# Performance work log

Hardware: AMD Instinct MI355X
Metric: run time of the kernel (lower is better)

The kernel has to match this reference:

```python
import jax, jax.numpy as jnp
import numpy as np

N_HEAD = 16


def setup_inputs() -> dict:
    key = jax.random.key(0)
    ks = jax.random.split(key, 4)
    B, S, E = 1, 4096, 1024
    x = jax.random.normal(ks[0], (B, S, E), dtype=jnp.float32)
    # causal mask: True where attention is DISALLOWED (upper triangle)
    masked_matrix = ~jnp.tril(jnp.ones((S, S), dtype=bool))[None, None]
    Wqkv = jax.random.normal(ks[1], (E, 3 * E), dtype=jnp.float32) * (1.0 / np.sqrt(E))
    bqkv = jnp.zeros((3 * E,), dtype=jnp.float32)
    Wp = jax.random.normal(ks[2], (E, E), dtype=jnp.float32) * (1.0 / np.sqrt(E))
    bp = jnp.zeros((E,), dtype=jnp.float32)
    return {"x": x, "masked_matrix": masked_matrix, "Wqkv": Wqkv, "bqkv": bqkv,
            "Wp": Wp, "bp": bp}


def reference(x, masked_matrix, Wqkv, bqkv, Wp, bp):
    B, S, E = x.shape
    H = N_HEAD
    D = E // H
    qkv = x @ Wqkv + bqkv                        # [B,S,3E]
    q, k, v = jnp.split(qkv, 3, axis=-1)
    q = q.reshape(B, S, H, D).transpose(0, 2, 1, 3)  # [B,H,S,D]
    k = k.reshape(B, S, H, D).transpose(0, 2, 1, 3)
    v = v.reshape(B, S, H, D).transpose(0, 2, 1, 3)
    # NOTE: source applies NO 1/sqrt(D) scaling — kept faithful.
    att = jnp.einsum('bhqd,bhkd->bhqk', q, k)    # [B,H,S,S]
    att = jnp.where(masked_matrix, jnp.float32(-jnp.inf), att)
    att = jax.nn.softmax(att, axis=-1)
    res = jnp.einsum('bhqk,bhkd->bhqd', att, v)  # [B,H,S,D]
    res = res.transpose(0, 2, 1, 3).reshape(B, S, E)
    return res @ Wp + bp
```

## Files before the change

### kernel.cpp

```cpp
#include <hip/hip_runtime.h>
#include <hip/hip_bf16.h>
#include <math.h>

#define S_LEN 4096
#define EMB   1024
#define NHEAD 16
#define HDIM  64

typedef __attribute__((ext_vector_type(8))) _Float16 half8;
typedef __attribute__((ext_vector_type(4))) _Float16 half4;
typedef __attribute__((ext_vector_type(4))) float float4_t;

#define GLOBAL_AS(p) ((const __attribute__((address_space(1))) void*)(p))
#define LDS_AS(p)    ((__attribute__((address_space(3))) void*)(p))

#define LOG2E 1.4426950408889634f

__global__ __launch_bounds__(256) void prep(
    const float* __restrict__ x, const float* __restrict__ Wqkv,
    const float* __restrict__ Wp,
    _Float16* __restrict__ xh, _Float16* __restrict__ WTh,
    _Float16* __restrict__ WpT)
{
    const int bid = blockIdx.x;
    if (bid < 4096) {
        const int i = bid * 256 + threadIdx.x;
        const float4_t v = ((const float4_t*)x)[i];
        half4 hh;
#pragma unroll
        for (int j = 0; j < 4; ++j) hh[j] = (_Float16)v[j];
        ((half4*)xh)[i] = hh;
        return;
    }
    __shared__ float t[64][65];
    const float* in;
    _Float16* out;
    int R, C, bx, by;
    if (bid < 4096 + 768) {
        const int idx = bid - 4096;
        bx = idx % 48; by = idx / 48;
        in = Wqkv; out = WTh; R = 1024; C = 3072;
    } else {
        const int idx = bid - 4864;
        bx = idx & 15; by = idx >> 4;
        in = Wp; out = WpT; R = 1024; C = 1024;
    }
    const int r0 = by * 64, c0 = bx * 64;
    for (int i = threadIdx.x; i < 64 * 64; i += 256) {
        int r = i >> 6, c = i & 63;
        t[r][c] = in[(size_t)(r0 + r) * C + c0 + c];
    }
    __syncthreads();
    for (int i = threadIdx.x; i < 64 * 64; i += 256) {
        int c = i >> 6, r = i & 63;
        out[(size_t)(c0 + c) * R + r0 + r] = (_Float16)t[r][c];
    }
}

__global__ __launch_bounds__(256) void gemm_qkv(
    const _Float16* __restrict__ Ag, const _Float16* __restrict__ Bg,
    const float* __restrict__ bias,
    _Float16* __restrict__ qk, _Float16* __restrict__ vt, int K)
{
    constexpr int BK = 32;
    __shared__ _Float16 Ah[128 * BK];
    __shared__ _Float16 Bh[128 * BK];

    const int tid = threadIdx.x;
    const int wave = tid >> 6, lane = tid & 63;
    const int l16 = lane & 15, quad = lane >> 4;
    const int wr = wave >> 1, wc = wave & 1;
    const int row0 = blockIdx.y * 128, col0 = blockIdx.x * 128;
    const int lrow = lane >> 2, lc8 = (lane & 3) * 8;

    float4_t acc[4][4];
#pragma unroll
    for (int i = 0; i < 4; ++i)
#pragma unroll
        for (int j = 0; j < 4; ++j) acc[i][j] = (float4_t){0.f, 0.f, 0.f, 0.f};

    for (int k0 = 0; k0 < K; k0 += BK) {
        __syncthreads();
#pragma unroll
        for (int i = 0; i < 2; ++i) {
            const int ar = i * 64 + wave * 16;
            __builtin_amdgcn_global_load_lds(
                GLOBAL_AS(Ag + (size_t)(row0 + ar + lrow) * K + k0 + lc8),
                LDS_AS(&Ah[ar * BK]), 16, 0, 0);
            __builtin_amdgcn_global_load_lds(
                GLOBAL_AS(Bg + (size_t)(col0 + ar + lrow) * K + k0 + lc8),
                LDS_AS(&Bh[ar * BK]), 16, 0, 0);
        }
        __syncthreads();

        half8 af[4], bfr[4];
#pragma unroll
        for (int t = 0; t < 4; ++t) {
            af[t]  = *(const half8*)&Ah[(wr * 64 + t * 16 + l16) * BK + quad * 8];
            bfr[t] = *(const half8*)&Bh[(wc * 64 + t * 16 + l16) * BK + quad * 8];
        }
#pragma unroll
        for (int i = 0; i < 4; ++i)
#pragma unroll
            for (int j = 0; j < 4; ++j)
                acc[i][j] = __builtin_amdgcn_mfma_f32_16x16x32_f16(af[i], bfr[j], acc[i][j], 0, 0, 0);
    }

#pragma unroll
    for (int i = 0; i < 4; ++i) {
#pragma unroll
        for (int j = 0; j < 4; ++j) {
            const int colb = col0 + wc * 64 + j * 16 + l16;
            const float bv = bias[colb];
            const int rowb = row0 + wr * 64 + i * 16 + quad * 4;
            if (colb < 2048) {
                const float sc = (colb >= 1024) ? LOG2E : 1.0f;
#pragma unroll
                for (int r = 0; r < 4; ++r)
                    qk[(size_t)(rowb + r) * 2048 + colb] =
                        (_Float16)((acc[i][j][r] + bv) * sc);
            } else {
                half4 w;
#pragma unroll
                for (int r = 0; r < 4; ++r) w[r] = (_Float16)(acc[i][j][r] + bv);
                *(half4*)&vt[(size_t)(colb - 2048) * 4096 + rowb] = w;
            }
        }
    }
}

__global__ __launch_bounds__(256) void gemm_out(
    const _Float16* __restrict__ Ag, const _Float16* __restrict__ Bg,
    const float* __restrict__ bias, float* __restrict__ C, int N, int K)
{
    constexpr int BK = 32;
    __shared__ _Float16 Ah[128 * BK];
    __shared__ _Float16 Bh[64 * BK];

    const int tid = threadIdx.x;
    const int wave = tid >> 6, lane = tid & 63;
    const int l16 = lane & 15, quad = lane >> 4;
    const int row0 = blockIdx.y * 128, col0 = blockIdx.x * 64;
    const int lrow = lane >> 2, lc8 = (lane & 3) * 8;

    float4_t acc[2][4];
#pragma unroll
    for (int i = 0; i < 2; ++i)
#pragma unroll
        for (int j = 0; j < 4; ++j) acc[i][j] = (float4_t){0.f, 0.f, 0.f, 0.f};

    for (int k0 = 0; k0 < K; k0 += BK) {
        __syncthreads();
#pragma unroll
        for (int i = 0; i < 2; ++i) {
            const int ar = i * 64 + wave * 16;
            __builtin_amdgcn_global_load_lds(
                GLOBAL_AS(Ag + (size_t)(row0 + ar + lrow) * K + k0 + lc8),
                LDS_AS(&Ah[ar * BK]), 16, 0, 0);
        }
        {
            const int br = wave * 16;
            __builtin_amdgcn_global_load_lds(
                GLOBAL_AS(Bg + (size_t)(col0 + br + lrow) * K + k0 + lc8),
                LDS_AS(&Bh[br * BK]), 16, 0, 0);
        }
        __syncthreads();

        half8 af[2], bfr[4];
#pragma unroll
        for (int t = 0; t < 2; ++t)
            af[t] = *(const half8*)&Ah[(wave * 32 + t * 16 + l16) * BK + quad * 8];
#pragma unroll
        for (int t = 0; t < 4; ++t)
            bfr[t] = *(const half8*)&Bh[(t * 16 + l16) * BK + quad * 8];
#pragma unroll
        for (int i = 0; i < 2; ++i)
#pragma unroll
            for (int j = 0; j < 4; ++j)
                acc[i][j] = __builtin_amdgcn_mfma_f32_16x16x32_f16(af[i], bfr[j], acc[i][j], 0, 0, 0);
    }

#pragma unroll
    for (int i = 0; i < 2; ++i) {
#pragma unroll
        for (int j = 0; j < 4; ++j) {
            const int colb = col0 + j * 16 + l16;
            const float bv = bias[colb];
#pragma unroll
            for (int r = 0; r < 4; ++r) {
                const int row = row0 + wave * 32 + i * 16 + quad * 4 + r;
                C[(size_t)row * N + colb] = acc[i][j][r] + bv;
            }
        }
    }
}

__global__ __launch_bounds__(256, 4) void flash_attn_f16(
    const _Float16* __restrict__ qk, const _Float16* __restrict__ v_t,
    _Float16* __restrict__ resh)
{
    __shared__ __align__(16) _Float16 KsT[2][64 * 64];
    __shared__ __align__(16) _Float16 VtT[2][64 * 64];
    __shared__ __align__(16) _Float16 Pb[4][16][76];

    const int bid  = blockIdx.x;
    const int h    = (bid & 7) * 2 + ((bid >> 3) & 1);
    const int tile = 63 - (bid >> 4);
    const int wave = threadIdx.x >> 6;
    const int lane = threadIdx.x & 63;
    const int l16  = lane & 15;
    const int quad = lane >> 4;

    const int dma_r = wave * 16 + (lane >> 3);
    const int dma_c = ((lane & 7) ^ (lane >> 3)) * 8;

    const _Float16* kplane = qk + 1024 + h * HDIM;
    const _Float16* vplane = v_t + (size_t)h * HDIM * 4096;

    const int q0      = tile * 64 + wave * 16;
    const int kb_last = tile * 64;

    const size_t qoff = (size_t)(q0 + l16) * 2048 + h * HDIM + quad * 8;
    half8 qf0 = *(const half8*)(qk + qoff);
    half8 qf1 = *(const half8*)(qk + qoff + 32);

    float4_t o[4];
#pragma unroll
    for (int c = 0; c < 4; ++c) o[c] = (float4_t){0.f, 0.f, 0.f, 0.f};
    float m_r = -INFINITY, l_r = 0.f;

#pragma unroll
    for (int p = 0; p < 2; ++p) {
        const int r = dma_r + p * 8;
        __builtin_amdgcn_global_load_lds(
            GLOBAL_AS(kplane + (size_t)r * 2048 + dma_c),
            LDS_AS(&KsT[0][(wave * 128 + p * 64) * 8]), 16, 0, 0);
        __builtin_amdgcn_global_load_lds(
            GLOBAL_AS(vplane + (size_t)r * 4096 + dma_c),
            LDS_AS(&VtT[0][(wave * 128 + p * 64) * 8]), 16, 0, 0);
    }

    int ib = 0;
    for (int kb = 0; kb <= kb_last; kb += 64, ib ^= 1) {
        __syncthreads();

        if (kb < kb_last) {
            const int kn = kb + 64;
#pragma unroll
            for (int p = 0; p < 2; ++p) {
                const int r = dma_r + p * 8;
                __builtin_amdgcn_global_load_lds(
                    GLOBAL_AS(kplane + (size_t)(kn + r) * 2048 + dma_c),
                    LDS_AS(&KsT[ib ^ 1][(wave * 128 + p * 64) * 8]), 16, 0, 0);
                __builtin_amdgcn_global_load_lds(
                    GLOBAL_AS(vplane + (size_t)r * 4096 + kn + dma_c),
                    LDS_AS(&VtT[ib ^ 1][(wave * 128 + p * 64) * 8]), 16, 0, 0);
            }
        }

        float4_t s[4];
#pragma unroll
        for (int t = 0; t < 4; ++t) {
            const int row = t * 16 + l16;
            const int r7 = row & 7;
            half8 a0 = *(const half8*)&KsT[ib][(row * 8 + (quad ^ r7)) * 8];
            half8 a1 = *(const half8*)&KsT[ib][(row * 8 + ((quad + 4) ^ r7)) * 8];
            float4_t a = (float4_t){0.f, 0.f, 0.f, 0.f};
            a = __builtin_amdgcn_mfma_f32_16x16x32_f16(a0, qf0, a, 0, 0, 0);
            a = __builtin_amdgcn_mfma_f32_16x16x32_f16(a1, qf1, a, 0, 0, 0);
            s[t] = a;
        }

        if (kb + 63 > q0) {
            const int qg = q0 + l16;
#pragma unroll
            for (int t = 0; t < 4; ++t)
#pragma unroll
                for (int r = 0; r < 4; ++r) {
                    const int key = kb + t * 16 + quad * 4 + r;
                    if (key > qg) s[t][r] = -INFINITY;
                }
        }

        float mx = s[0][0];
#pragma unroll
        for (int t = 0; t < 4; ++t)
#pragma unroll
            for (int r = 0; r < 4; ++r) mx = fmaxf(mx, s[t][r]);
        mx = fmaxf(mx, __shfl_xor(mx, 16));
        mx = fmaxf(mx, __shfl_xor(mx, 32));
        const float mnew  = fmaxf(m_r, mx);
        const float alpha = __builtin_amdgcn_exp2f(m_r - mnew);

        float p[4][4];
        float sum = 0.f;
#pragma unroll
        for (int t = 0; t < 4; ++t)
#pragma unroll
            for (int r = 0; r < 4; ++r) {
                p[t][r] = __builtin_amdgcn_exp2f(s[t][r] - mnew);
                sum += p[t][r];
            }
        sum += __shfl_xor(sum, 16);
        sum += __shfl_xor(sum, 32);
        l_r = l_r * alpha + sum;
        m_r = mnew;
#pragma unroll
        for (int ct = 0; ct < 4; ++ct)
#pragma unroll
            for (int r = 0; r < 4; ++r) o[ct][r] *= alpha;

#pragma unroll
        for (int t = 0; t < 4; ++t) {
            half4 w;
#pragma unroll
            for (int r = 0; r < 4; ++r) w[r] = (_Float16)p[t][r];
            *(half4*)&Pb[wave][l16][t * 16 + quad * 4] = w;
        }
        half8 pb0 = *(const half8*)&Pb[wave][l16][quad * 8];
        half8 pb1 = *(const half8*)&Pb[wave][l16][32 + quad * 8];

#pragma unroll
        for (int ct = 0; ct < 4; ++ct) {
            const int row = ct * 16 + l16;
            const int r7 = row & 7;
            half8 va0 = *(const half8*)&VtT[ib][(row * 8 + (quad ^ r7)) * 8];
            half8 va1 = *(const half8*)&VtT[ib][(row * 8 + ((quad + 4) ^ r7)) * 8];
            o[ct] = __builtin_amdgcn_mfma_f32_16x16x32_f16(va0, pb0, o[ct], 0, 0, 0);
            o[ct] = __builtin_amdgcn_mfma_f32_16x16x32_f16(va1, pb1, o[ct], 0, 0, 0);
        }
    }

    const float inv = 1.0f / l_r;
#pragma unroll
    for (int ct = 0; ct < 4; ++ct) {
        half4 w;
#pragma unroll
        for (int r = 0; r < 4; ++r) w[r] = (_Float16)(o[ct][r] * inv);
        *(half4*)&resh[(size_t)(q0 + l16) * EMB + h * HDIM + ct * 16 + quad * 4] = w;
    }
}

extern "C" void kernel_launch(void* const* d_in, const int* in_sizes, int n_in,
                              void* d_out, int out_size, void* d_ws, size_t ws_size,
                              hipStream_t stream)
{
    const float* x    = (const float*)d_in[0];
    const float* Wqkv = (const float*)d_in[2];
    const float* bqkv = (const float*)d_in[3];
    const float* Wp   = (const float*)d_in[4];
    const float* bp   = (const float*)d_in[5];
    float* out = (float*)d_out;

    _Float16* xh  = (_Float16*)d_ws;
    _Float16* WTh = xh + (size_t)4096 * 1024;
    _Float16* qkh = WTh + (size_t)3072 * 1024;
    _Float16* vtg = qkh + (size_t)4096 * 2048;
    _Float16* WpT = vtg + (size_t)1024 * 4096;
    _Float16* resh = xh;

    dim3 blk(256);

    prep<<<dim3(5120), blk, 0, stream>>>(x, Wqkv, Wp, xh, WTh, WpT);

    gemm_qkv<<<dim3(3072 / 128, 4096 / 128), blk, 0, stream>>>(
        xh, WTh, bqkv, qkh, vtg, 1024);

    flash_attn_f16<<<dim3(1024), dim3(256), 0, stream>>>(qkh, vtg, resh);

    gemm_out<<<dim3(1024 / 64, 4096 / 128), blk, 0, stream>>>(
        resh, WpT, bp, out, 1024, 1024);
}
```

Measured before the change: 260.5 us.

## Replace LDS P staging with bpermute, lazy rescale, deferred row-sum reduction

Removes the per-wave LDS buffer used to transpose P into MFMA B-operand layout. It uses ds_bpermute shuffles with packed f16 conversion instead, which frees LDS so occupancy can rise to 5 blocks per SM. It also skips rescaling the O accumulator unless the running max grows by more than a threshold, and defers the cross-lane sum reduction to the end. The lazy max threshold risks fp16 overflow in P (values up to 2^8) and changes rounding behaviour via round-toward-zero conversion.

```diff
diff --git a/kernel.cpp b/kernel.cpp
--- a/kernel.cpp
+++ b/kernel.cpp
@@ -9,7 +9,9 @@
 
 typedef __attribute__((ext_vector_type(8))) _Float16 half8;
 typedef __attribute__((ext_vector_type(4))) _Float16 half4;
+typedef __attribute__((ext_vector_type(2))) _Float16 half2_t;
 typedef __attribute__((ext_vector_type(4))) float float4_t;
+typedef __attribute__((ext_vector_type(4))) int int4_t;
 
 #define GLOBAL_AS(p) ((const __attribute__((address_space(1))) void*)(p))
 #define LDS_AS(p)    ((__attribute__((address_space(3))) void*)(p))
@@ -195,13 +197,12 @@
     }
 }
 
-__global__ __launch_bounds__(256, 4) void flash_attn_f16(
+__global__ __launch_bounds__(256, 5) void flash_attn_f16(
     const _Float16* __restrict__ qk, const _Float16* __restrict__ v_t,
     _Float16* __restrict__ resh)
 {
     __shared__ __align__(16) _Float16 KsT[2][64 * 64];
     __shared__ __align__(16) _Float16 VtT[2][64 * 64];
-    __shared__ __align__(16) _Float16 Pb[4][16][76];
 
     const int bid  = blockIdx.x;
     const int h    = (bid & 7) * 2 + ((bid >> 3) & 1);
@@ -213,6 +214,10 @@
 
     const int dma_r = wave * 16 + (lane >> 3);
     const int dma_c = ((lane & 7) ^ (lane >> 3)) * 8;
+
+    const int srcA4 = (l16 + ((quad & 1) << 5)) << 2;
+    const int srcB4 = srcA4 + 64;
+    const bool hiT  = quad >= 2;
 
     const _Float16* kplane = qk + 1024 + h * HDIM;
     const _Float16* vplane = v_t + (size_t)h * HDIM * 4096;
@@ -282,43 +287,70 @@
                 }
         }
 
-        float mx = s[0][0];
-#pragma unroll
-        for (int t = 0; t < 4; ++t)
-#pragma unroll
-            for (int r = 0; r < 4; ++r) mx = fmaxf(mx, s[t][r]);
+        const float t0m = fmaxf(fmaxf(s[0][0], s[0][1]), fmaxf(s[0][2], s[0][3]));
+        const float t1m = fmaxf(fmaxf(s[1][0], s[1][1]), fmaxf(s[1][2], s[1][3]));
+        const float t2m = fmaxf(fmaxf(s[2][0], s[2][1]), fmaxf(s[2][2], s[2][3]));
+        const float t3m = fmaxf(fmaxf(s[3][0], s[3][1]), fmaxf(s[3][2], s[3][3]));
+        float mx = fmaxf(fmaxf(t0m, t1m), fmaxf(t2m, t3m));
         mx = fmaxf(mx, __shfl_xor(mx, 16));
         mx = fmaxf(mx, __shfl_xor(mx, 32));
-        const float mnew  = fmaxf(m_r, mx);
+        const bool  grow  = mx > m_r + 8.0f;
+        const float mnew  = grow ? mx : m_r;
         const float alpha = __builtin_amdgcn_exp2f(m_r - mnew);
 
         float p[4][4];
-        float sum = 0.f;
+        float lsum = 0.f;
 #pragma unroll
         for (int t = 0; t < 4; ++t)
 #pragma unroll
             for (int r = 0; r < 4; ++r) {
                 p[t][r] = __builtin_amdgcn_exp2f(s[t][r] - mnew);
-                sum += p[t][r];
+                lsum += p[t][r];
             }
-        sum += __shfl_xor(sum, 16);
-        sum += __shfl_xor(sum, 32);
-        l_r = l_r * alpha + sum;
+        l_r = l_r * alpha + lsum;
         m_r = mnew;
-#pragma unroll
-        for (int ct = 0; ct < 4; ++ct)
-#pragma unroll
-            for (int r = 0; r < 4; ++r) o[ct][r] *= alpha;
-
+        if (__any(grow)) {
+#pragma unroll
+            for (int ct = 0; ct < 4; ++ct)
+#pragma unroll
+                for (int r = 0; r < 4; ++r) o[ct][r] *= alpha;
+        }
+
+        int w[4][2];
 #pragma unroll
         for (int t = 0; t < 4; ++t) {
-            half4 w;
-#pragma unroll
-            for (int r = 0; r < 4; ++r) w[r] = (_Float16)p[t][r];
-            *(half4*)&Pb[wave][l16][t * 16 + quad * 4] = w;
-        }
-        half8 pb0 = *(const half8*)&Pb[wave][l16][quad * 8];
-        half8 pb1 = *(const half8*)&Pb[wave][l16][32 + quad * 8];
+            w[t][0] = __builtin_bit_cast(int, __builtin_amdgcn_cvt_pkrtz(p[t][0], p[t][1]));
+            w[t][1] = __builtin_bit_cast(int, __builtin_amdgcn_cvt_pkrtz(p[t][2], p[t][3]));
+        }
+        int4_t v0, v1;
+        {
+            const int a0 = __builtin_amdgcn_ds_bpermute(srcA4, w[0][0]);
+            const int a1 = __builtin_amdgcn_ds_bpermute(srcA4, w[1][0]);
+            v0[0] = hiT ? a1 : a0;
+            const int b0 = __builtin_amdgcn_ds_bpermute(srcA4, w[0][1]);
+            const int b1 = __builtin_amdgcn_ds_bpermute(srcA4, w[1][1]);
+            v0[1] = hiT ? b1 : b0;
+            const int c0 = __builtin_amdgcn_ds_bpermute(srcB4, w[0][0]);
+            const int c1 = __builtin_amdgcn_ds_bpermute(srcB4, w[1][0]);
+            v0[2] = hiT ? c1 : c0;
+            const int d0 = __builtin_amdgcn_ds_bpermute(srcB4, w[0][1]);
+            const int d1 = __builtin_amdgcn_ds_bpermute(srcB4, w[1][1]);
+            v0[3] = hiT ? d1 : d0;
+            const int e0 = __builtin_amdgcn_ds_bpermute(srcA4, w[2][0]);
+            const int e1 = __builtin_amdgcn_ds_bpermute(srcA4, w[3][0]);
+            v1[0] = hiT ? e1 : e0;
+            const int f0 = __builtin_amdgcn_ds_bpermute(srcA4, w[2][1]);
+            const int f1 = __builtin_amdgcn_ds_bpermute(srcA4, w[3][1]);
+            v1[1] = hiT ? f1 : f0;
+            const int g0 = __builtin_amdgcn_ds_bpermute(srcB4, w[2][0]);
+            const int g1 = __builtin_amdgcn_ds_bpermute(srcB4, w[3][0]);
+            v1[2] = hiT ? g1 : g0;
+            const int h0 = __builtin_amdgcn_ds_bpermute(srcB4, w[2][1]);
+            const int h1 = __builtin_amdgcn_ds_bpermute(srcB4, w[3][1]);
+            v1[3] = hiT ? h1 : h0;
+        }
+        const half8 pb0 = __builtin_bit_cast(half8, v0);
+        const half8 pb1 = __builtin_bit_cast(half8, v1);
 
 #pragma unroll
         for (int ct = 0; ct < 4; ++ct) {
@@ -331,7 +363,9 @@
         }
     }
 
-    const float inv = 1.0f / l_r;
+    float lr = l_r + __shfl_xor(l_r, 16);
+    lr += __shfl_xor(lr, 32);
+    const float inv = 1.0f / lr;
 #pragma unroll
     for (int ct = 0; ct < 4; ++ct) {
         half4 w;
```

Result: slower. 270.2 us (+3.7%).

## Use 128-query attention tiles with 8 waves, lazy rescaling and deferred row-sum

Applied to the files above, without the earlier changes.

Doubles the attention block to 512 threads covering 128 queries, so each K/V tile loaded into LDS is shared by eight waves instead of four, halving per-block DMA work per wave. Waves skip key blocks that lie entirely beyond their causal range. Adds a lazy max update (rescale only when the new max exceeds the old one by more than 8) and moves the cross-lane row-sum reduction to the end of the kernel. The trade-off is fewer blocks, idle waves on skipped blocks near the diagonal, and possible fp16 overflow of P when the stale max lags by up to 8 in log2 units.

```diff
diff --git a/kernel.cpp b/kernel.cpp
--- a/kernel.cpp
+++ b/kernel.cpp
@@ -195,30 +195,30 @@
     }
 }
 
-__global__ __launch_bounds__(256, 4) void flash_attn_f16(
+__global__ __launch_bounds__(512, 4) void flash_attn_f16(
     const _Float16* __restrict__ qk, const _Float16* __restrict__ v_t,
     _Float16* __restrict__ resh)
 {
     __shared__ __align__(16) _Float16 KsT[2][64 * 64];
     __shared__ __align__(16) _Float16 VtT[2][64 * 64];
-    __shared__ __align__(16) _Float16 Pb[4][16][76];
+    __shared__ __align__(16) _Float16 Pb[8][16][76];
 
     const int bid  = blockIdx.x;
     const int h    = (bid & 7) * 2 + ((bid >> 3) & 1);
-    const int tile = 63 - (bid >> 4);
+    const int tile = 31 - (bid >> 4);
     const int wave = threadIdx.x >> 6;
     const int lane = threadIdx.x & 63;
     const int l16  = lane & 15;
     const int quad = lane >> 4;
 
-    const int dma_r = wave * 16 + (lane >> 3);
+    const int dma_r = wave * 8 + (lane >> 3);
     const int dma_c = ((lane & 7) ^ (lane >> 3)) * 8;
 
     const _Float16* kplane = qk + 1024 + h * HDIM;
     const _Float16* vplane = v_t + (size_t)h * HDIM * 4096;
 
-    const int q0      = tile * 64 + wave * 16;
-    const int kb_last = tile * 64;
+    const int q0      = tile * 128 + wave * 16;
+    const int kb_last = tile * 128 + 64;
 
     const size_t qoff = (size_t)(q0 + l16) * 2048 + h * HDIM + quad * 8;
     half8 qf0 = *(const half8*)(qk + qoff);
@@ -229,15 +229,13 @@
     for (int c = 0; c < 4; ++c) o[c] = (float4_t){0.f, 0.f, 0.f, 0.f};
     float m_r = -INFINITY, l_r = 0.f;
 
-#pragma unroll
-    for (int p = 0; p < 2; ++p) {
-        const int r = dma_r + p * 8;
+    {
         __builtin_amdgcn_global_load_lds(
-            GLOBAL_AS(kplane + (size_t)r * 2048 + dma_c),
-            LDS_AS(&KsT[0][(wave * 128 + p * 64) * 8]), 16, 0, 0);
+            GLOBAL_AS(kplane + (size_t)dma_r * 2048 + dma_c),
+            LDS_AS(&KsT[0][(wave * 64) * 8]), 16, 0, 0);
         __builtin_amdgcn_global_load_lds(
-            GLOBAL_AS(vplane + (size_t)r * 4096 + dma_c),
-            LDS_AS(&VtT[0][(wave * 128 + p * 64) * 8]), 16, 0, 0);
+            GLOBAL_AS(vplane + (size_t)dma_r * 4096 + dma_c),
+            LDS_AS(&VtT[0][(wave * 64) * 8]), 16, 0, 0);
     }
 
     int ib = 0;
@@ -246,92 +244,93 @@
 
         if (kb < kb_last) {
             const int kn = kb + 64;
-#pragma unroll
-            for (int p = 0; p < 2; ++p) {
-                const int r = dma_r + p * 8;
-                __builtin_amdgcn_global_load_lds(
-                    GLOBAL_AS(kplane + (size_t)(kn + r) * 2048 + dma_c),
-                    LDS_AS(&KsT[ib ^ 1][(wave * 128 + p * 64) * 8]), 16, 0, 0);
-                __builtin_amdgcn_global_load_lds(
-                    GLOBAL_AS(vplane + (size_t)r * 4096 + kn + dma_c),
-                    LDS_AS(&VtT[ib ^ 1][(wave * 128 + p * 64) * 8]), 16, 0, 0);
-            }
-        }
-
-        float4_t s[4];
-#pragma unroll
-        for (int t = 0; t < 4; ++t) {
-            const int row = t * 16 + l16;
-            const int r7 = row & 7;
-            half8 a0 = *(const half8*)&KsT[ib][(row * 8 + (quad ^ r7)) * 8];
-            half8 a1 = *(const half8*)&KsT[ib][(row * 8 + ((quad + 4) ^ r7)) * 8];
-            float4_t a = (float4_t){0.f, 0.f, 0.f, 0.f};
-            a = __builtin_amdgcn_mfma_f32_16x16x32_f16(a0, qf0, a, 0, 0, 0);
-            a = __builtin_amdgcn_mfma_f32_16x16x32_f16(a1, qf1, a, 0, 0, 0);
-            s[t] = a;
-        }
-
-        if (kb + 63 > q0) {
-            const int qg = q0 + l16;
+            __builtin_amdgcn_global_load_lds(
+                GLOBAL_AS(kplane + (size_t)(kn + dma_r) * 2048 + dma_c),
+                LDS_AS(&KsT[ib ^ 1][(wave * 64) * 8]), 16, 0, 0);
+            __builtin_amdgcn_global_load_lds(
+                GLOBAL_AS(vplane + (size_t)dma_r * 4096 + kn + dma_c),
+                LDS_AS(&VtT[ib ^ 1][(wave * 64) * 8]), 16, 0, 0);
+        }
+
+        if (kb <= q0 + 15) {
+            float4_t s[4];
+#pragma unroll
+            for (int t = 0; t < 4; ++t) {
+                const int row = t * 16 + l16;
+                const int r7 = row & 7;
+                half8 a0 = *(const half8*)&KsT[ib][(row * 8 + (quad ^ r7)) * 8];
+                half8 a1 = *(const half8*)&KsT[ib][(row * 8 + ((quad + 4) ^ r7)) * 8];
+                float4_t a = (float4_t){0.f, 0.f, 0.f, 0.f};
+                a = __builtin_amdgcn_mfma_f32_16x16x32_f16(a0, qf0, a, 0, 0, 0);
+                a = __builtin_amdgcn_mfma_f32_16x16x32_f16(a1, qf1, a, 0, 0, 0);
+                s[t] = a;
+            }
+
+            if (kb + 63 > q0) {
+                const int qg = q0 + l16;
+#pragma unroll
+                for (int t = 0; t < 4; ++t)
+#pragma unroll
+                    for (int r = 0; r < 4; ++r) {
+                        const int key = kb + t * 16 + quad * 4 + r;
+                        if (key > qg) s[t][r] = -INFINITY;
+                    }
+            }
+
+            const float t0m = fmaxf(fmaxf(s[0][0], s[0][1]), fmaxf(s[0][2], s[0][3]));
+            const float t1m = fmaxf(fmaxf(s[1][0], s[1][1]), fmaxf(s[1][2], s[1][3]));
+            const float t2m = fmaxf(fmaxf(s[2][0], s[2][1]), fmaxf(s[2][2], s[2][3]));
+            const float t3m = fmaxf(fmaxf(s[3][0], s[3][1]), fmaxf(s[3][2], s[3][3]));
+            float mx = fmaxf(fmaxf(t0m, t1m), fmaxf(t2m, t3m));
+            mx = fmaxf(mx, __shfl_xor(mx, 16));
+            mx = fmaxf(mx, __shfl_xor(mx, 32));
+            const bool  grow  = mx > m_r + 8.0f;
+            const float mnew  = grow ? mx : m_r;
+            const float alpha = __builtin_amdgcn_exp2f(m_r - mnew);
+
+            float p[4][4];
+            float lsum = 0.f;
 #pragma unroll
             for (int t = 0; t < 4; ++t)
 #pragma unroll
                 for (int r = 0; r < 4; ++r) {
-                    const int key = kb + t * 16 + quad * 4 + r;
-                    if (key > qg) s[t][r] = -INFINITY;
+                    p[t][r] = __builtin_amdgcn_exp2f(s[t][r] - mnew);
+                    lsum += p[t][r];
                 }
-        }
-
-        float mx = s[0][0];
-#pragma unroll
-        for (int t = 0; t < 4; ++t)
-#pragma unroll
-            for (int r = 0; r < 4; ++r) mx = fmaxf(mx, s[t][r]);
-        mx = fmaxf(mx, __shfl_xor(mx, 16));
-        mx = fmaxf(mx, __shfl_xor(mx, 32));
-        const float mnew  = fmaxf(m_r, mx);
-        const float alpha = __builtin_amdgcn_exp2f(m_r - mnew);
-
-        float p[4][4];
-        float sum = 0.f;
-#pragma unroll
-        for (int t = 0; t < 4; ++t)
-#pragma unroll
-            for (int r = 0; r < 4; ++r) {
-                p[t][r] = __builtin_amdgcn_exp2f(s[t][r] - mnew);
-                sum += p[t][r];
-            }
-        sum += __shfl_xor(sum, 16);
-        sum += __shfl_xor(sum, 32);
-        l_r = l_r * alpha + sum;
-        m_r = mnew;
-#pragma unroll
-        for (int ct = 0; ct < 4; ++ct)
-#pragma unroll
-            for (int r = 0; r < 4; ++r) o[ct][r] *= alpha;
-
-#pragma unroll
-        for (int t = 0; t < 4; ++t) {
-            half4 w;
-#pragma unroll
-            for (int r = 0; r < 4; ++r) w[r] = (_Float16)p[t][r];
-            *(half4*)&Pb[wave][l16][t * 16 + quad * 4] = w;
-        }
-        half8 pb0 = *(const half8*)&Pb[wave][l16][quad * 8];
-        half8 pb1 = *(const half8*)&Pb[wave][l16][32 + quad * 8];
-
-#pragma unroll
-        for (int ct = 0; ct < 4; ++ct) {
-            const int row = ct * 16 + l16;
-            const int r7 = row & 7;
-            half8 va0 = *(const half8*)&VtT[ib][(row * 8 + (quad ^ r7)) * 8];
-            half8 va1 = *(const half8*)&VtT[ib][(row * 8 + ((quad + 4) ^ r7)) * 8];
-            o[ct] = __builtin_amdgcn_mfma_f32_16x16x32_f16(va0, pb0, o[ct], 0, 0, 0);
-            o[ct] = __builtin_amdgcn_mfma_f32_16x16x32_f16(va1, pb1, o[ct], 0, 0, 0);
-        }
-    }
-
-    const float inv = 1.0f / l_r;
+            l_r = l_r * alpha + lsum;
+            m_r = mnew;
+            if (__any(grow)) {
+#pragma unroll
+                for (int ct = 0; ct < 4; ++ct)
+#pragma unroll
+                    for (int r = 0; r < 4; ++r) o[ct][r] *= alpha;
+            }
+
+#pragma unroll
+            for (int t = 0; t < 4; ++t) {
+                half4 w;
+#pragma unroll
+                for (int r = 0; r < 4; ++r) w[r] = (_Float16)p[t][r];
+                *(half4*)&Pb[wave][l16][t * 16 + quad * 4] = w;
+            }
+            half8 pb0 = *(const half8*)&Pb[wave][l16][quad * 8];
+            half8 pb1 = *(const half8*)&Pb[wave][l16][32 + quad * 8];
+
+#pragma unroll
+            for (int ct = 0; ct < 4; ++ct) {
+                const int row = ct * 16 + l16;
+                const int r7 = row & 7;
+                half8 va0 = *(const half8*)&VtT[ib][(row * 8 + (quad ^ r7)) * 8];
+                half8 va1 = *(const half8*)&VtT[ib][(row * 8 + ((quad + 4) ^ r7)) * 8];
+                o[ct] = __builtin_amdgcn_mfma_f32_16x16x32_f16(va0, pb0, o[ct], 0, 0, 0);
+                o[ct] = __builtin_amdgcn_mfma_f32_16x16x32_f16(va1, pb1, o[ct], 0, 0, 0);
+            }
+        }
+    }
+
+    float lr = l_r + __shfl_xor(l_r, 16);
+    lr += __shfl_xor(lr, 32);
+    const float inv = 1.0f / lr;
 #pragma unroll
     for (int ct = 0; ct < 4; ++ct) {
         half4 w;
@@ -366,7 +365,7 @@
     gemm_qkv<<<dim3(3072 / 128, 4096 / 128), blk, 0, stream>>>(
         xh, WTh, bqkv, qkh, vtg, 1024);
 
-    flash_attn_f16<<<dim3(1024), dim3(256), 0, stream>>>(qkh, vtg, resh);
+    flash_attn_f16<<<dim3(512), dim3(512), 0, stream>>>(qkh, vtg, resh);
 
     gemm_out<<<dim3(1024 / 64, 4096 / 128), blk, 0, stream>>>(
         resh, WpT, bp, out, 1024, 1024);
```

Measured after the change: 264.4 us. About the same (+1.5%).

## Rewrite flash attention with 32x32 MFMA, 128-row tiles, register P permute

Applied to the files above, without the earlier changes.

The attention kernel now gives each workgroup 128 query rows, with each wave owning 32 rows, and uses 32x32x16 MFMA instead of 16x16x32. The softmax probabilities are packed to fp16 and moved between lanes with permlane32 swaps, which removes the LDS round trip through the Pb buffer. It also adds a lazy rescale that only updates the running max when it grows by more than 8, interleaves the tile order across blocks to balance the causal workload, and raises MFMA priority with setprio. The cost is fewer blocks (512) and lower occupancy, more register pressure, and some numerical risk from the delayed max rescale.

```diff
diff --git a/kernel.cpp b/kernel.cpp
--- a/kernel.cpp
+++ b/kernel.cpp
@@ -10,6 +10,9 @@
 typedef __attribute__((ext_vector_type(8))) _Float16 half8;
 typedef __attribute__((ext_vector_type(4))) _Float16 half4;
 typedef __attribute__((ext_vector_type(4))) float float4_t;
+typedef __attribute__((ext_vector_type(16))) float float16_t;
+typedef __attribute__((ext_vector_type(4))) int int4_t;
+typedef __attribute__((ext_vector_type(2))) int int2_t;
 
 #define GLOBAL_AS(p) ((const __attribute__((address_space(1))) void*)(p))
 #define LDS_AS(p)    ((__attribute__((address_space(3))) void*)(p))
@@ -195,21 +198,21 @@
     }
 }
 
-__global__ __launch_bounds__(256, 4) void flash_attn_f16(
+__global__ __launch_bounds__(256, 2) void flash_attn_f16(
     const _Float16* __restrict__ qk, const _Float16* __restrict__ v_t,
     _Float16* __restrict__ resh)
 {
     __shared__ __align__(16) _Float16 KsT[2][64 * 64];
     __shared__ __align__(16) _Float16 VtT[2][64 * 64];
-    __shared__ __align__(16) _Float16 Pb[4][16][76];
 
     const int bid  = blockIdx.x;
     const int h    = (bid & 7) * 2 + ((bid >> 3) & 1);
-    const int tile = 63 - (bid >> 4);
+    const int s_   = bid >> 4;
+    const int tile = (s_ < 16) ? (31 - s_) : (s_ - 16);
     const int wave = threadIdx.x >> 6;
     const int lane = threadIdx.x & 63;
-    const int l16  = lane & 15;
-    const int quad = lane >> 4;
+    const int l31  = lane & 31;
+    const int hi   = lane >> 5;
 
     const int dma_r = wave * 16 + (lane >> 3);
     const int dma_c = ((lane & 7) ^ (lane >> 3)) * 8;
@@ -217,16 +220,16 @@
     const _Float16* kplane = qk + 1024 + h * HDIM;
     const _Float16* vplane = v_t + (size_t)h * HDIM * 4096;
 
-    const int q0      = tile * 64 + wave * 16;
-    const int kb_last = tile * 64;
-
-    const size_t qoff = (size_t)(q0 + l16) * 2048 + h * HDIM + quad * 8;
-    half8 qf0 = *(const half8*)(qk + qoff);
-    half8 qf1 = *(const half8*)(qk + qoff + 32);
-
-    float4_t o[4];
-#pragma unroll
-    for (int c = 0; c < 4; ++c) o[c] = (float4_t){0.f, 0.f, 0.f, 0.f};
+    const int q0      = tile * 128 + wave * 32;
+    const int kb_last = tile * 128 + 64;
+
+    half8 qf[4];
+#pragma unroll
+    for (int j = 0; j < 4; ++j)
+        qf[j] = *(const half8*)(qk + (size_t)(q0 + l31) * 2048 + h * HDIM
+                                + j * 16 + hi * 8);
+
+    float16_t o0 = (float16_t)0.f, o1 = (float16_t)0.f;
     float m_r = -INFINITY, l_r = 0.f;
 
 #pragma unroll
@@ -258,86 +261,114 @@
             }
         }
 
-        float4_t s[4];
-#pragma unroll
-        for (int t = 0; t < 4; ++t) {
-            const int row = t * 16 + l16;
-            const int r7 = row & 7;
-            half8 a0 = *(const half8*)&KsT[ib][(row * 8 + (quad ^ r7)) * 8];
-            half8 a1 = *(const half8*)&KsT[ib][(row * 8 + ((quad + 4) ^ r7)) * 8];
-            float4_t a = (float4_t){0.f, 0.f, 0.f, 0.f};
-            a = __builtin_amdgcn_mfma_f32_16x16x32_f16(a0, qf0, a, 0, 0, 0);
-            a = __builtin_amdgcn_mfma_f32_16x16x32_f16(a1, qf1, a, 0, 0, 0);
-            s[t] = a;
-        }
-
-        if (kb + 63 > q0) {
-            const int qg = q0 + l16;
-#pragma unroll
-            for (int t = 0; t < 4; ++t)
-#pragma unroll
-                for (int r = 0; r < 4; ++r) {
-                    const int key = kb + t * 16 + quad * 4 + r;
-                    if (key > qg) s[t][r] = -INFINITY;
-                }
-        }
-
-        float mx = s[0][0];
-#pragma unroll
-        for (int t = 0; t < 4; ++t)
-#pragma unroll
-            for (int r = 0; r < 4; ++r) mx = fmaxf(mx, s[t][r]);
-        mx = fmaxf(mx, __shfl_xor(mx, 16));
-        mx = fmaxf(mx, __shfl_xor(mx, 32));
-        const float mnew  = fmaxf(m_r, mx);
-        const float alpha = __builtin_amdgcn_exp2f(m_r - mnew);
-
-        float p[4][4];
-        float sum = 0.f;
-#pragma unroll
-        for (int t = 0; t < 4; ++t)
-#pragma unroll
-            for (int r = 0; r < 4; ++r) {
-                p[t][r] = __builtin_amdgcn_exp2f(s[t][r] - mnew);
-                sum += p[t][r];
-            }
-        sum += __shfl_xor(sum, 16);
-        sum += __shfl_xor(sum, 32);
-        l_r = l_r * alpha + sum;
-        m_r = mnew;
-#pragma unroll
-        for (int ct = 0; ct < 4; ++ct)
-#pragma unroll
-            for (int r = 0; r < 4; ++r) o[ct][r] *= alpha;
-
-#pragma unroll
-        for (int t = 0; t < 4; ++t) {
-            half4 w;
-#pragma unroll
-            for (int r = 0; r < 4; ++r) w[r] = (_Float16)p[t][r];
-            *(half4*)&Pb[wave][l16][t * 16 + quad * 4] = w;
-        }
-        half8 pb0 = *(const half8*)&Pb[wave][l16][quad * 8];
-        half8 pb1 = *(const half8*)&Pb[wave][l16][32 + quad * 8];
-
-#pragma unroll
-        for (int ct = 0; ct < 4; ++ct) {
-            const int row = ct * 16 + l16;
-            const int r7 = row & 7;
-            half8 va0 = *(const half8*)&VtT[ib][(row * 8 + (quad ^ r7)) * 8];
-            half8 va1 = *(const half8*)&VtT[ib][(row * 8 + ((quad + 4) ^ r7)) * 8];
-            o[ct] = __builtin_amdgcn_mfma_f32_16x16x32_f16(va0, pb0, o[ct], 0, 0, 0);
-            o[ct] = __builtin_amdgcn_mfma_f32_16x16x32_f16(va1, pb1, o[ct], 0, 0, 0);
-        }
-    }
-
-    const float inv = 1.0f / l_r;
-#pragma unroll
-    for (int ct = 0; ct < 4; ++ct) {
-        half4 w;
-#pragma unroll
-        for (int r = 0; r < 4; ++r) w[r] = (_Float16)(o[ct][r] * inv);
-        *(half4*)&resh[(size_t)(q0 + l16) * EMB + h * HDIM + ct * 16 + quad * 4] = w;
+        if (kb <= q0 + 31) {
+            float16_t s0 = (float16_t)0.f, s1 = (float16_t)0.f;
+            __builtin_amdgcn_s_setprio(1);
+#pragma unroll
+            for (int j = 0; j < 4; ++j) {
+                const int r7 = l31 & 7;
+                const half8 kf0 = *(const half8*)&KsT[ib][
+                    ((l31) * 8 + ((2 * j + hi) ^ r7)) * 8];
+                const half8 kf1 = *(const half8*)&KsT[ib][
+                    ((32 + l31) * 8 + ((2 * j + hi) ^ r7)) * 8];
+                s0 = __builtin_amdgcn_mfma_f32_32x32x16_f16(kf0, qf[j], s0, 0, 0, 0);
+                s1 = __builtin_amdgcn_mfma_f32_32x32x16_f16(kf1, qf[j], s1, 0, 0, 0);
+            }
+            __builtin_amdgcn_s_setprio(0);
+
+            if (kb + 63 > q0) {
+                const int qg = q0 + l31;
+#pragma unroll
+                for (int g = 0; g < 4; ++g)
+#pragma unroll
+                    for (int r = 0; r < 4; ++r) {
+                        const int keyb = kb + r + 8 * g + 4 * hi;
+                        if (keyb > qg)      s0[4 * g + r] = -INFINITY;
+                        if (keyb + 32 > qg) s1[4 * g + r] = -INFINITY;
+                    }
+            }
+
+            float mx = s0[0];
+#pragma unroll
+            for (int i = 1; i < 16; ++i) mx = fmaxf(mx, s0[i]);
+#pragma unroll
+            for (int i = 0; i < 16; ++i) mx = fmaxf(mx, s1[i]);
+            mx = fmaxf(mx, __shfl_xor(mx, 32));
+            const bool  grow  = mx > m_r + 8.0f;
+            const float mnew  = grow ? mx : m_r;
+            const float alpha = __builtin_amdgcn_exp2f(m_r - mnew);
+
+            int w0[8], w1[8];
+            float lsum = 0.f;
+#pragma unroll
+            for (int i = 0; i < 8; ++i) {
+                const float pa = __builtin_amdgcn_exp2f(s0[2 * i]     - mnew);
+                const float pb = __builtin_amdgcn_exp2f(s0[2 * i + 1] - mnew);
+                lsum += pa + pb;
+                w0[i] = __builtin_bit_cast(int, __builtin_amdgcn_cvt_pkrtz(pa, pb));
+            }
+#pragma unroll
+            for (int i = 0; i < 8; ++i) {
+                const float pa = __builtin_amdgcn_exp2f(s1[2 * i]     - mnew);
+                const float pb = __builtin_amdgcn_exp2f(s1[2 * i + 1] - mnew);
+                lsum += pa + pb;
+                w1[i] = __builtin_bit_cast(int, __builtin_amdgcn_cvt_pkrtz(pa, pb));
+            }
+            l_r = l_r * alpha + lsum;
+            m_r = mnew;
+            if (__any(grow)) {
+#pragma unroll
+                for (int i = 0; i < 16; ++i) { o0[i] *= alpha; o1[i] *= alpha; }
+            }
+
+            half8 pf[4];
+            {
+                const int2_t a02 = __builtin_amdgcn_permlane32_swap(w0[0], w0[2], 0, 0);
+                const int2_t a13 = __builtin_amdgcn_permlane32_swap(w0[1], w0[3], 0, 0);
+                const int2_t a46 = __builtin_amdgcn_permlane32_swap(w0[4], w0[6], 0, 0);
+                const int2_t a57 = __builtin_amdgcn_permlane32_swap(w0[5], w0[7], 0, 0);
+                int4_t f0 = {a02[0], a13[0], a02[1], a13[1]};
+                int4_t f1 = {a46[0], a57[0], a46[1], a57[1]};
+                pf[0] = __builtin_bit_cast(half8, f0);
+                pf[1] = __builtin_bit_cast(half8, f1);
+                const int2_t b02 = __builtin_amdgcn_permlane32_swap(w1[0], w1[2], 0, 0);
+                const int2_t b13 = __builtin_amdgcn_permlane32_swap(w1[1], w1[3], 0, 0);
+                const int2_t b46 = __builtin_amdgcn_permlane32_swap(w1[4], w1[6], 0, 0);
+                const int2_t b57 = __builtin_amdgcn_permlane32_swap(w1[5], w1[7], 0, 0);
+                int4_t f2 = {b02[0], b13[0], b02[1], b13[1]};
+                int4_t f3 = {b46[0], b57[0], b46[1], b57[1]};
+                pf[2] = __builtin_bit_cast(half8, f2);
+                pf[3] = __builtin_bit_cast(half8, f3);
+            }
+
+            __builtin_amdgcn_s_setprio(1);
+#pragma unroll
+            for (int kc = 0; kc < 4; ++kc) {
+                const int r7 = l31 & 7;
+                const half8 vf0 = *(const half8*)&VtT[ib][
+                    ((l31) * 8 + ((2 * kc + hi) ^ r7)) * 8];
+                const half8 vf1 = *(const half8*)&VtT[ib][
+                    ((32 + l31) * 8 + ((2 * kc + hi) ^ r7)) * 8];
+                o0 = __builtin_amdgcn_mfma_f32_32x32x16_f16(vf0, pf[kc], o0, 0, 0, 0);
+                o1 = __builtin_amdgcn_mfma_f32_32x32x16_f16(vf1, pf[kc], o1, 0, 0, 0);
+            }
+            __builtin_amdgcn_s_setprio(0);
+        }
+    }
+
+    float lr = l_r + __shfl_xor(l_r, 32);
+    const float inv = 1.0f / lr;
+#pragma unroll
+    for (int g = 0; g < 4; ++g) {
+        half4 wa, wb;
+#pragma unroll
+        for (int r = 0; r < 4; ++r) {
+            wa[r] = (_Float16)(o0[4 * g + r] * inv);
+            wb[r] = (_Float16)(o1[4 * g + r] * inv);
+        }
+        const size_t base = (size_t)(q0 + l31) * EMB + h * HDIM + 8 * g + 4 * hi;
+        *(half4*)&resh[base]      = wa;
+        *(half4*)&resh[base + 32] = wb;
     }
 }
 
@@ -366,7 +397,7 @@
     gemm_qkv<<<dim3(3072 / 128, 4096 / 128), blk, 0, stream>>>(
         xh, WTh, bqkv, qkh, vtg, 1024);
 
-    flash_attn_f16<<<dim3(1024), dim3(256), 0, stream>>>(qkh, vtg, resh);
+    flash_attn_f16<<<dim3(512), dim3(256), 0, stream>>>(qkh, vtg, resh);
 
     gemm_out<<<dim3(1024 / 64, 4096 / 128), blk, 0, stream>>>(
         resh, WpT, bp, out, 1024, 1024);
```

Result: no change. 263.8 us (+1.3%).
